# Performance work log

Hardware: AMD Instinct MI355X
Metric: run time of the kernel (lower is better)

Reference implementation:

```python
import jax, jax.numpy as jnp
import numpy as np

EPS = 1e-4          # ReEig epsilon buffer
IN_SIZE = 4096      # input SPD matrix is IN_SIZE x IN_SIZE
HID = 5             # hard-coded bottleneck in RiemSPD
OUT_SIZE = 2048     # output SPD matrix is OUT_SIZE x OUT_SIZE


def _orthogonal(key, rows, cols):
    # mimic nn.init.orthogonal_: semi-orthogonal (rows, cols) matrix
    n, m = max(rows, cols), min(rows, cols)
    a = jax.random.normal(key, (n, m), dtype=jnp.float32)
    q, _ = jnp.linalg.qr(a)
    q = q[:, :m]
    return q if rows >= cols else q.T


def bimap(x, w):
    # BiMap.forward: W^T @ X @ W
    return w.T @ (x @ w)


def rectify(x):
    # Rectify.forward: SVD, clip singular values at EPS, rebuild u diag(s) u^T
    u, s, _ = jnp.linalg.svd(x)
    s = jnp.maximum(s, EPS)
    return (u * s[None, :]) @ u.T


def setup_inputs() -> dict:
    key = jax.random.key(0)
    k1, k2, k3 = jax.random.split(key, 3)
    X = jax.random.normal(k1, (1, IN_SIZE, IN_SIZE), dtype=jnp.float32)
    W1 = _orthogonal(k2, IN_SIZE, HID)   # encoder BiMap weight (in_size, 5)
    W2 = _orthogonal(k3, HID, OUT_SIZE)  # decoder BiMap weight (5, out_size)
    return {"X": X, "W1": W1, "W2": W2}


def reference(X, W1, W2):
    x = X[0]                       # squeeze(0): (IN_SIZE, IN_SIZE)
    y = rectify(bimap(x, W1))      # encoder: (5, 5)
    z = rectify(bimap(y, W2))      # decoder: (OUT_SIZE, OUT_SIZE)
    return z
```

## Files before the change

kernel.cpp:

```cpp
#include <hip/hip_runtime.h>
#include <math.h>

static constexpr int N   = 4096;
static constexpr int H   = 5;
static constexpr int NO  = 2048;
static constexpr float FEPS = 1e-4f;
static constexpr int RPB  = 8;
static constexpr int NBLK = N / RPB;
static constexpr int NR   = 8;

#if __has_builtin(__builtin_amdgcn_rcpf)
__device__ __forceinline__ float frcp(float x) { return __builtin_amdgcn_rcpf(x); }
#else
__device__ __forceinline__ float frcp(float x) { return 1.0f / x; }
#endif
#if __has_builtin(__builtin_amdgcn_rsqf)
__device__ __forceinline__ float frsq(float x) { return __builtin_amdgcn_rsqf(x); }
#else
__device__ __forceinline__ float frsq(float x) { return 1.0f / sqrtf(x); }
#endif

__device__ __forceinline__ float wave_reduce(float v) {
#pragma unroll
    for (int o = 32; o > 0; o >>= 1) v += __shfl_down(v, o, 64);
    return v;
}

__global__ __launch_bounds__(256) void k_xw1(const float* __restrict__ X,
                                             const float* __restrict__ W1,
                                             float* __restrict__ Mp) {
    const int rb = blockIdx.x * RPB;
    const int t  = threadIdx.x;
    const float4* W14 = reinterpret_cast<const float4*>(W1);

    float acc[RPB][H];
#pragma unroll
    for (int r = 0; r < RPB; ++r)
#pragma unroll
        for (int a = 0; a < H; ++a) acc[r][a] = 0.f;

#pragma unroll
    for (int c = 0; c < 4; ++c) {
        const int j4 = c * 256 + t;
        float wf[20];
        {
            const float4 f0 = W14[5 * j4 + 0];
            const float4 f1 = W14[5 * j4 + 1];
            const float4 f2 = W14[5 * j4 + 2];
            const float4 f3 = W14[5 * j4 + 3];
            const float4 f4 = W14[5 * j4 + 4];
            wf[0]=f0.x;  wf[1]=f0.y;  wf[2]=f0.z;  wf[3]=f0.w;
            wf[4]=f1.x;  wf[5]=f1.y;  wf[6]=f1.z;  wf[7]=f1.w;
            wf[8]=f2.x;  wf[9]=f2.y;  wf[10]=f2.z; wf[11]=f2.w;
            wf[12]=f3.x; wf[13]=f3.y; wf[14]=f3.z; wf[15]=f3.w;
            wf[16]=f4.x; wf[17]=f4.y; wf[18]=f4.z; wf[19]=f4.w;
        }
#pragma unroll
        for (int r = 0; r < RPB; ++r) {
            const float4 x = reinterpret_cast<const float4*>(
                                 X + (size_t)(rb + r) * N)[j4];
#pragma unroll
            for (int a = 0; a < H; ++a)
                acc[r][a] += x.x * wf[a]      + x.y * wf[5 + a]
                           + x.z * wf[10 + a] + x.w * wf[15 + a];
        }
    }

    float m[H][H];
#pragma unroll
    for (int a = 0; a < H; ++a)
#pragma unroll
        for (int b = 0; b < H; ++b) m[a][b] = 0.f;
#pragma unroll
    for (int r = 0; r < RPB; ++r) {
        float w1r[H];
#pragma unroll
        for (int a = 0; a < H; ++a) w1r[a] = W1[(size_t)(rb + r) * H + a];
#pragma unroll
        for (int a = 0; a < H; ++a)
#pragma unroll
            for (int b = 0; b < H; ++b) m[a][b] += w1r[a] * acc[r][b];
    }

    __shared__ float sm[4][25];
    const int lane = t & 63, wv = t >> 6;
#pragma unroll
    for (int a = 0; a < H; ++a)
#pragma unroll
        for (int b = 0; b < H; ++b) {
            const float v = wave_reduce(m[a][b]);
            if (lane == 0) sm[wv][a * H + b] = v;
        }
    __syncthreads();
    if (t < 25)
        Mp[blockIdx.x * 25 + t] = sm[0][t] + sm[1][t] + sm[2][t] + sm[3][t];
}

#define JROT(p, q)                                                            \
    {                                                                         \
        const float apq = __shfl(a, (p) * 5 + (q), 64);                       \
        const float app = __shfl(a, (p) * 5 + (p), 64);                       \
        const float aqq = __shfl(a, (q) * 5 + (q), 64);                       \
        const bool  skip =                                                    \
            (apq * apq) <= (1e-26f * (app * app + aqq * aqq) + 1e-38f);       \
        const float theta = (aqq - app) * frcp(2.0f * apq);                   \
        const float tden  = fabsf(theta) + sqrtf(theta * theta + 1.0f);       \
        const float ttv   = ((theta >= 0.0f) ? 1.0f : -1.0f) * frcp(tden);    \
        float cc = frsq(ttv * ttv + 1.0f);                                    \
        float ss = ttv * cc;                                                  \
        cc = skip ? 1.0f : cc;                                                \
        ss = skip ? 0.0f : ss;                                                \
        {                                                                     \
            const int  pr   = ((r == (p)) ? (q) : ((r == (q)) ? (p) : r));    \
            const float prt = __shfl(a, pr * 5 + c, 64);                      \
            a = (r == (p)) ? (cc * a - ss * prt)                              \
                           : ((r == (q)) ? (ss * prt + cc * a) : a);          \
        }                                                                     \
        {                                                                     \
            const int  pc   = ((c == (p)) ? (q) : ((c == (q)) ? (p) : c));    \
            const float prt = __shfl(a, r * 5 + pc, 64);                      \
            a = (c == (p)) ? (cc * a - ss * prt)                              \
                           : ((c == (q)) ? (ss * prt + cc * a) : a);          \
            const float urt = __shfl(u, r * 5 + pc, 64);                      \
            u = (c == (p)) ? (cc * u - ss * urt)                              \
                           : ((c == (q)) ? (ss * urt + cc * u) : u);          \
        }                                                                     \
    }

__global__ __launch_bounds__(256) void k_out(const float* __restrict__ Mp,
                                             const float* __restrict__ W2,
                                             float* __restrict__ Z) {
    __shared__ float sred[10][26];
    __shared__ float Msum[25];
    __shared__ float ys[25];
    const int t = threadIdx.x;

    if (t < 250) {
        const int e = t % 25, g = t / 25;
        float s = 0.f;
#pragma unroll 8
        for (int p = g; p < NBLK; p += 10) s += Mp[p * 25 + e];
        sred[g][e] = s;
    }
    __syncthreads();
    if (t < 25) {
        float s = 0.f;
#pragma unroll
        for (int g = 0; g < 10; ++g) s += sred[g][t];
        Msum[t] = s;
    }
    __syncthreads();

    if (t < 64) {
        const int r = t / 5, c = t % 5;
        const float m = (t < 25) ? Msum[t] : 0.f;
        float a = 0.f;
#pragma unroll
        for (int k = 0; k < H; ++k)
            a += __shfl(m, r * 5 + k, 64) * __shfl(m, c * 5 + k, 64);
        float u = (t < 25 && r == c) ? 1.0f : 0.0f;

        for (int sweep = 0; sweep < 6; ++sweep) {
            JROT(0, 1) JROT(0, 2) JROT(0, 3) JROT(0, 4) JROT(1, 2)
            JROT(1, 3) JROT(1, 4) JROT(2, 3) JROT(2, 4) JROT(3, 4)
        }

        const float ev = fmaxf(sqrtf(fmaxf(a, 0.0f)), FEPS);
        float yv = 0.f;
#pragma unroll
        for (int k = 0; k < H; ++k) {
            const float evk = __shfl(ev, 6 * k, 64);
            const float urk = __shfl(u, r * 5 + k, 64);
            const float uck = __shfl(u, c * 5 + k, 64);
            yv += evk * urk * uck;
        }
        if (t < 25) ys[t] = yv - ((r == c) ? FEPS : 0.f);
    }
    __syncthreads();

    const int i0 = blockIdx.x * NR;
    float cmat[NR][H];
#pragma unroll
    for (int r = 0; r < NR; ++r) {
        float wcol[H];
#pragma unroll
        for (int k = 0; k < H; ++k) wcol[k] = W2[(size_t)k * NO + i0 + r];
#pragma unroll
        for (int m = 0; m < H; ++m) {
            float s = 0.f;
#pragma unroll
            for (int k = 0; k < H; ++k) s += wcol[k] * ys[k * H + m];
            cmat[r][m] = s;
        }
    }

#pragma unroll
    for (int hh = 0; hh < 2; ++hh) {
        const int jj = (hh * 256 + t) * 4;
        float4 w2j[H];
#pragma unroll
        for (int m = 0; m < H; ++m)
            w2j[m] = *reinterpret_cast<const float4*>(W2 + (size_t)m * NO + jj);
#pragma unroll
        for (int r = 0; r < NR; ++r) {
            const int i = i0 + r;
            float zx = 0.f, zy = 0.f, zz = 0.f, zw = 0.f;
#pragma unroll
            for (int m = 0; m < H; ++m) {
                const float cm = cmat[r][m];
                zx += cm * w2j[m].x;
                zy += cm * w2j[m].y;
                zz += cm * w2j[m].z;
                zw += cm * w2j[m].w;
            }
            if (i >= jj && i < jj + 4) {
                if      (i == jj + 0) zx += FEPS;
                else if (i == jj + 1) zy += FEPS;
                else if (i == jj + 2) zz += FEPS;
                else                  zw += FEPS;
            }
            *reinterpret_cast<float4*>(Z + (size_t)i * NO + jj) =
                make_float4(zx, zy, zz, zw);
        }
    }
}

extern "C" void kernel_launch(void* const* d_in, const int* in_sizes, int n_in,
                              void* d_out, int out_size, void* d_ws, size_t ws_size,
                              hipStream_t stream) {
    const float* X  = (const float*)d_in[0];
    const float* W1 = (const float*)d_in[1];
    const float* W2 = (const float*)d_in[2];
    float* out = (float*)d_out;
    float* ws  = (float*)d_ws;

    float* Mp = ws;

    hipLaunchKernelGGL(k_xw1, dim3(NBLK),    dim3(256), 0, stream, X, W1, Mp);
    hipLaunchKernelGGL(k_out, dim3(NO / NR), dim3(256), 0, stream, Mp, W2, out);
}
```

Before: 43.95 us.

## Fuse producer and consumer kernels into one launch with atomic semaphore

Merges the X·W1 reduction kernel and the output kernel into a single launch. The first NBLK blocks write partial 5x5 products and increment a global counter, and the remaining 256 blocks spin on that counter before building the output. This removes one kernel launch and the gap between the two kernels. In exchange it adds a memset, atomic traffic and spinning consumer blocks, and it relies on all producer blocks being scheduled before consumers fill the device, which is a deadlock risk in principle.

```diff
diff --git a/kernel.cpp b/kernel.cpp
--- a/kernel.cpp
+++ b/kernel.cpp
@@ -5,9 +5,10 @@
 static constexpr int H   = 5;
 static constexpr int NO  = 2048;
 static constexpr float FEPS = 1e-4f;
-static constexpr int RPB  = 8;
-static constexpr int NBLK = N / RPB;
-static constexpr int NR   = 8;
+static constexpr int RPB   = 8;
+static constexpr int NBLK  = N / RPB;
+static constexpr int NCONS = 256;
+static constexpr int NR    = NO / NCONS;
 
 #if __has_builtin(__builtin_amdgcn_rcpf)
 __device__ __forceinline__ float frcp(float x) { return __builtin_amdgcn_rcpf(x); }
@@ -24,76 +25,6 @@
 #pragma unroll
     for (int o = 32; o > 0; o >>= 1) v += __shfl_down(v, o, 64);
     return v;
-}
-
-__global__ __launch_bounds__(256) void k_xw1(const float* __restrict__ X,
-                                             const float* __restrict__ W1,
-                                             float* __restrict__ Mp) {
-    const int rb = blockIdx.x * RPB;
-    const int t  = threadIdx.x;
-    const float4* W14 = reinterpret_cast<const float4*>(W1);
-
-    float acc[RPB][H];
-#pragma unroll
-    for (int r = 0; r < RPB; ++r)
-#pragma unroll
-        for (int a = 0; a < H; ++a) acc[r][a] = 0.f;
-
-#pragma unroll
-    for (int c = 0; c < 4; ++c) {
-        const int j4 = c * 256 + t;
-        float wf[20];
-        {
-            const float4 f0 = W14[5 * j4 + 0];
-            const float4 f1 = W14[5 * j4 + 1];
-            const float4 f2 = W14[5 * j4 + 2];
-            const float4 f3 = W14[5 * j4 + 3];
-            const float4 f4 = W14[5 * j4 + 4];
-            wf[0]=f0.x;  wf[1]=f0.y;  wf[2]=f0.z;  wf[3]=f0.w;
-            wf[4]=f1.x;  wf[5]=f1.y;  wf[6]=f1.z;  wf[7]=f1.w;
-            wf[8]=f2.x;  wf[9]=f2.y;  wf[10]=f2.z; wf[11]=f2.w;
-            wf[12]=f3.x; wf[13]=f3.y; wf[14]=f3.z; wf[15]=f3.w;
-            wf[16]=f4.x; wf[17]=f4.y; wf[18]=f4.z; wf[19]=f4.w;
-        }
-#pragma unroll
-        for (int r = 0; r < RPB; ++r) {
-            const float4 x = reinterpret_cast<const float4*>(
-                                 X + (size_t)(rb + r) * N)[j4];
-#pragma unroll
-            for (int a = 0; a < H; ++a)
-                acc[r][a] += x.x * wf[a]      + x.y * wf[5 + a]
-                           + x.z * wf[10 + a] + x.w * wf[15 + a];
-        }
-    }
-
-    float m[H][H];
-#pragma unroll
-    for (int a = 0; a < H; ++a)
-#pragma unroll
-        for (int b = 0; b < H; ++b) m[a][b] = 0.f;
-#pragma unroll
-    for (int r = 0; r < RPB; ++r) {
-        float w1r[H];
-#pragma unroll
-        for (int a = 0; a < H; ++a) w1r[a] = W1[(size_t)(rb + r) * H + a];
-#pragma unroll
-        for (int a = 0; a < H; ++a)
-#pragma unroll
-            for (int b = 0; b < H; ++b) m[a][b] += w1r[a] * acc[r][b];
-    }
-
-    __shared__ float sm[4][25];
-    const int lane = t & 63, wv = t >> 6;
-#pragma unroll
-    for (int a = 0; a < H; ++a)
-#pragma unroll
-        for (int b = 0; b < H; ++b) {
-            const float v = wave_reduce(m[a][b]);
-            if (lane == 0) sm[wv][a * H + b] = v;
-        }
-    __syncthreads();
-    if (t < 25)
-        Mp[blockIdx.x * 25 + t] = sm[0][t] + sm[1][t] + sm[2][t] + sm[3][t];
 }
 
 #define JROT(p, q)                                                            \
@@ -127,19 +58,112 @@
         }                                                                     \
     }
 
-__global__ __launch_bounds__(256) void k_out(const float* __restrict__ Mp,
-                                             const float* __restrict__ W2,
-                                             float* __restrict__ Z) {
+__global__ __launch_bounds__(256, 2) void k_fused(const float* __restrict__ X,
+                                                  const float* __restrict__ W1,
+                                                  const float* __restrict__ W2,
+                                                  float* __restrict__ Z,
+                                                  float* __restrict__ Mp,
+                                                  unsigned int* __restrict__ sem) {
+    const int t = threadIdx.x;
+
+    if (blockIdx.x < NBLK) {
+        const int b  = blockIdx.x;
+        const int rb = b * RPB;
+        const float4* W14 = reinterpret_cast<const float4*>(W1);
+
+        float acc[RPB][H];
+#pragma unroll
+        for (int r = 0; r < RPB; ++r)
+#pragma unroll
+            for (int a = 0; a < H; ++a) acc[r][a] = 0.f;
+
+#pragma unroll
+        for (int c = 0; c < 4; ++c) {
+            const int j4 = c * 256 + t;
+            float wf[20];
+            {
+                const float4 f0 = W14[5 * j4 + 0];
+                const float4 f1 = W14[5 * j4 + 1];
+                const float4 f2 = W14[5 * j4 + 2];
+                const float4 f3 = W14[5 * j4 + 3];
+                const float4 f4 = W14[5 * j4 + 4];
+                wf[0]=f0.x;  wf[1]=f0.y;  wf[2]=f0.z;  wf[3]=f0.w;
+                wf[4]=f1.x;  wf[5]=f1.y;  wf[6]=f1.z;  wf[7]=f1.w;
+                wf[8]=f2.x;  wf[9]=f2.y;  wf[10]=f2.z; wf[11]=f2.w;
+                wf[12]=f3.x; wf[13]=f3.y; wf[14]=f3.z; wf[15]=f3.w;
+                wf[16]=f4.x; wf[17]=f4.y; wf[18]=f4.z; wf[19]=f4.w;
+            }
+#pragma unroll
+            for (int r = 0; r < RPB; ++r) {
+                const float4 x = reinterpret_cast<const float4*>(
+                                     X + (size_t)(rb + r) * N)[j4];
+#pragma unroll
+                for (int a = 0; a < H; ++a)
+                    acc[r][a] += x.x * wf[a]      + x.y * wf[5 + a]
+                               + x.z * wf[10 + a] + x.w * wf[15 + a];
+            }
+        }
+
+        float pm[H][H];
+#pragma unroll
+        for (int a = 0; a < H; ++a)
+#pragma unroll
+            for (int bb = 0; bb < H; ++bb) pm[a][bb] = 0.f;
+#pragma unroll
+        for (int r = 0; r < RPB; ++r) {
+            float w1r[H];
+#pragma unroll
+            for (int a = 0; a < H; ++a) w1r[a] = W1[(size_t)(rb + r) * H + a];
+#pragma unroll
+            for (int a = 0; a < H; ++a)
+#pragma unroll
+                for (int bb = 0; bb < H; ++bb) pm[a][bb] += w1r[a] * acc[r][bb];
+        }
+
+        __shared__ float sm[4][25];
+        {
+            const int lane = t & 63, wv = t >> 6;
+#pragma unroll
+            for (int a = 0; a < H; ++a)
+#pragma unroll
+                for (int bb = 0; bb < H; ++bb) {
+                    const float v = wave_reduce(pm[a][bb]);
+                    if (lane == 0) sm[wv][a * H + bb] = v;
+                }
+        }
+        __syncthreads();
+        if (t < 25) {
+            const float v = sm[0][t] + sm[1][t] + sm[2][t] + sm[3][t];
+            __hip_atomic_store(&Mp[b * 25 + t], v, __ATOMIC_RELAXED,
+                               __HIP_MEMORY_SCOPE_AGENT);
+        }
+        __syncthreads();
+        if (t == 0) {
+            __threadfence();
+            __hip_atomic_fetch_add(sem, 1u, __ATOMIC_RELEASE,
+                                   __HIP_MEMORY_SCOPE_AGENT);
+        }
+        return;
+    }
+
+    if (t == 0) {
+        while (__hip_atomic_load(sem, __ATOMIC_ACQUIRE,
+                                 __HIP_MEMORY_SCOPE_AGENT) < (unsigned)NBLK)
+            __builtin_amdgcn_s_sleep(2);
+    }
+    __syncthreads();
+    __threadfence();
+
     __shared__ float sred[10][26];
     __shared__ float Msum[25];
     __shared__ float ys[25];
-    const int t = threadIdx.x;
 
     if (t < 250) {
         const int e = t % 25, g = t / 25;
         float s = 0.f;
-#pragma unroll 8
-        for (int p = g; p < NBLK; p += 10) s += Mp[p * 25 + e];
+        for (int p = g; p < NBLK; p += 10)
+            s += __hip_atomic_load(&Mp[p * 25 + e], __ATOMIC_RELAXED,
+                                   __HIP_MEMORY_SCOPE_AGENT);
         sred[g][e] = s;
     }
     __syncthreads();
@@ -178,7 +202,7 @@
     }
     __syncthreads();
 
-    const int i0 = blockIdx.x * NR;
+    const int i0 = (blockIdx.x - NBLK) * NR;
     float cmat[NR][H];
 #pragma unroll
     for (int r = 0; r < NR; ++r) {
@@ -235,7 +259,9 @@
     float* ws  = (float*)d_ws;
 
     float* Mp = ws;
-
-    hipLaunchKernelGGL(k_xw1, dim3(NBLK),    dim3(256), 0, stream, X, W1, Mp);
-    hipLaunchKernelGGL(k_out, dim3(NO / NR), dim3(256), 0, stream, Mp, W2, out);
+    unsigned int* sem = (unsigned int*)(ws + NBLK * 25);
+
+    (void)hipMemsetAsync(sem, 0, sizeof(unsigned int), stream);
+    hipLaunchKernelGGL(k_fused, dim3(NBLK + NCONS), dim3(256), 0, stream,
+                       X, W1, W2, out, Mp, sem);
 }
```

New measurement: 90.64 us. 106% more time.
